# Kernel optimization log

Measured on AMD Instinct MI355X. Metric: run time of the kernel, lower is better.

Reference implementation:

```python
import jax, jax.numpy as jnp
import numpy as np

QC = 12          # effective quantum channels (quantum_channels//4*4)
G = 3            # number of 4-channel quantum groups
DIM = 128
NGROUPS_GN = 8
NUM_LAYER = 1

# PauliZ sign table: wire 0 is the most-significant qubit (PennyLane default.qubit)
_SIGNS = np.array([[1.0 - 2.0 * ((k >> (3 - w)) & 1) for w in range(4)]
                   for k in range(16)], dtype=np.float32)


def _apply_rx(state, phi, w):
    # state: [B,2,2,2,2] complex64; phi: [B]; RX = cos(p/2) I - i sin(p/2) X
    c = jnp.cos(0.5 * phi).astype(jnp.complex64)
    s = (-1j) * jnp.sin(0.5 * phi).astype(jnp.complex64)
    U = jnp.stack([jnp.stack([c, s], -1), jnp.stack([s, c], -1)], -2)  # [B,2,2]
    st = jnp.moveaxis(state, 1 + w, -1)
    st = jnp.einsum('bij,b...j->b...i', U, st)
    return jnp.moveaxis(st, -1, 1 + w)


def _apply_cnot(state, c, t):
    st = jnp.moveaxis(state, (1 + c, 1 + t), (-2, -1))
    st = jnp.concatenate([st[..., 0:1, :], st[..., 1:2, ::-1]], axis=-2)
    return jnp.moveaxis(st, (-2, -1), (1 + c, 1 + t))


def _circuit(x4, theta):
    # AngleEmbedding(RX) + NUM_LAYER x Basic_ansatz; x4: [B,4], theta: [4*NUM_LAYER]
    B = x4.shape[0]
    state = jnp.zeros((B, 2, 2, 2, 2), jnp.complex64).at[:, 0, 0, 0, 0].set(1.0)
    for w in range(4):
        state = _apply_rx(state, x4[:, w], w)
    for l in range(NUM_LAYER):
        th = theta[4 * l:4 * (l + 1)]
        for w in range(4):
            state = _apply_rx(state, jnp.broadcast_to(th[w], (B,)), w)
        for c in range(3):
            state = _apply_cnot(state, c, c + 1)
        state = _apply_cnot(state, 3, 0)
    probs = jnp.abs(state.reshape(B, 16)) ** 2
    return probs @ jnp.asarray(_SIGNS)  # [B,4] PauliZ expvals


def _quantum_block(x_q, qparams):
    # x_q: [B,H,W,QC]; pool spatially, run per-group circuit, broadcast back
    B, H, W, Cq = x_q.shape
    pooled = jnp.mean(x_q, axis=(1, 2)).reshape(B, Cq // 4, 4)
    y = jax.vmap(_circuit, in_axes=(1, 0), out_axes=1)(pooled, qparams)  # [B,G,4]
    y = y.reshape(B, 1, 1, Cq)
    return jnp.broadcast_to(y, (B, H, W, Cq))


def _ws_conv(x, kernel, bias):
    eps = 1e-5  # fp32 branch of WeightStandardizedConv
    mean = jnp.mean(kernel, axis=(0, 1, 2), keepdims=True)
    var = jnp.var(kernel, axis=(0, 1, 2), keepdims=True)
    k = (kernel - mean) / jnp.sqrt(var + eps)
    y = jax.lax.conv_general_dilated(x, k, (1, 1), ((1, 1), (1, 1)),
                                     dimension_numbers=('NHWC', 'HWIO', 'NHWC'))
    return y + bias


def _group_norm(x, scale, bias, groups=NGROUPS_GN, eps=1e-6):
    B, H, W, C = x.shape
    xg = x.reshape(B, H, W, groups, C // groups)
    mu = jnp.mean(xg, axis=(1, 2, 4), keepdims=True)
    var = jnp.var(xg, axis=(1, 2, 4), keepdims=True)
    xn = ((xg - mu) / jnp.sqrt(var + eps)).reshape(B, H, W, C)
    return xn * scale + bias


def setup_inputs() -> dict:
    key = jax.random.key(0)
    ks = jax.random.split(key, 8)
    B, H, W, C, T = 16, 64, 64, DIM, 512
    cc = DIM - QC  # classical conv channels = 116
    return {
        'x': jax.random.normal(ks[0], (B, H, W, C), jnp.float32),
        'time_emb': jax.random.normal(ks[1], (B, T), jnp.float32),
        'qparams': jax.random.uniform(ks[2], (G, 4), jnp.float32),
        'conv0_kernel': jax.random.normal(ks[3], (3, 3, cc, cc), jnp.float32) * 0.05,
        'conv0_bias': jnp.zeros((cc,), jnp.float32),
        'conv1_kernel': jax.random.normal(ks[4], (3, 3, cc, cc), jnp.float32) * 0.05,
        'conv1_bias': jnp.zeros((cc,), jnp.float32),
        'gn0_scale': jnp.ones((C,), jnp.float32),
        'gn0_bias': jnp.zeros((C,), jnp.float32),
        'gn1_scale': jnp.ones((C,), jnp.float32),
        'gn1_bias': jnp.zeros((C,), jnp.float32),
        'time_w': jax.random.normal(ks[5], (T, 2 * DIM), jnp.float32) * 0.02,
        'time_b': jnp.zeros((2 * DIM,), jnp.float32),
    }


def reference(x, time_emb, qparams, conv0_kernel, conv0_bias, conv1_kernel,
              conv1_bias, gn0_scale, gn0_bias, gn1_scale, gn1_bias, time_w, time_b):
    # first quantum + classical branch
    h_q = _quantum_block(x[..., :QC], qparams)
    h_c = _ws_conv(x[..., QC:], conv0_kernel, conv0_bias)
    h = jnp.concatenate([h_q, h_c], axis=-1)
    h = _group_norm(h, gn0_scale, gn0_bias)
    # FiLM conditioning from time embedding
    t = jax.nn.swish(time_emb) @ time_w + time_b  # [B, 2*DIM]
    scale, shift = jnp.split(t[:, None, None, :], 2, axis=-1)
    h = jax.nn.swish(h * (1 + scale) + shift)
    # second quantum + classical branch
    h_q2 = _quantum_block(h[..., :QC], qparams)
    h_c2 = _ws_conv(h[..., QC:], conv1_kernel, conv1_bias)
    h2 = jnp.concatenate([h_q2, h_c2], axis=-1)
    h2 = jax.nn.swish(_group_norm(h2, gn1_scale, gn1_bias))
    return x + h2
```

## Files before the change

kernel.cpp:

```cpp
#include <hip/hip_runtime.h>
#include <math.h>

#define BATCH 16
#define NPX 4096
#define CDIM 128
#define CC 116
#define KTAPS 1044

using u16 = unsigned short;
typedef __attribute__((ext_vector_type(8))) short short8;
typedef __attribute__((ext_vector_type(16))) float f32x16;

__device__ __forceinline__ float swishf(float z) {
    return z / (1.f + __expf(-z));
}
__device__ __forceinline__ float bf2f(u16 u) {
    union { unsigned int i; float f; } v; v.i = ((unsigned int)u) << 16; return v.f;
}
__device__ __forceinline__ u16 f2bf(float f) {
    union { float f; unsigned int i; } v; v.f = f;
    unsigned int r = v.i + 0x7fffu + ((v.i >> 16) & 1u);
    return (u16)(r >> 16);
}

__global__ void k_pre(const float* __restrict__ x, float* __restrict__ part,
                      float* __restrict__ csums) {
    const int bx = blockIdx.x, tid = threadIdx.x;
    if (bx >= 128) {
        int i = (bx - 128) * 256 + tid;
        csums[i * 2] = 0.f;
        csums[i * 2 + 1] = 0.f;
        return;
    }
    const int b = bx >> 3, seg = bx & 7;
    float s[12];
#pragma unroll
    for (int c = 0; c < 12; ++c) s[c] = 0.f;
    const float* xb = x + (size_t)(b * 4096 + seg * 512) * CDIM;
#pragma unroll
    for (int i = 0; i < 2; ++i) {
        const float4* p = (const float4*)(xb + (size_t)(tid + i * 256) * CDIM);
        float4 v0 = p[0], v1 = p[1], v2 = p[2];
        s[0] += v0.x; s[1] += v0.y; s[2] += v0.z; s[3] += v0.w;
        s[4] += v1.x; s[5] += v1.y; s[6] += v1.z; s[7] += v1.w;
        s[8] += v2.x; s[9] += v2.y; s[10] += v2.z; s[11] += v2.w;
    }
    __shared__ float red[12][256];
#pragma unroll
    for (int c = 0; c < 12; ++c) red[c][tid] = s[c];
    __syncthreads();
    for (int st = 128; st > 0; st >>= 1) {
        if (tid < st) {
#pragma unroll
            for (int c = 0; c < 12; ++c) red[c][tid] += red[c][tid + st];
        }
        __syncthreads();
    }
    if (tid < 12) part[bx * 12 + tid] = red[tid][0];
}

__device__ void run_circuit(const float* ang, const float* th, float* z) {
    float ar[16], ai[16];
#pragma unroll
    for (int k = 0; k < 16; ++k) { ar[k] = 0.f; ai[k] = 0.f; }
    ar[0] = 1.f;
#pragma unroll
    for (int pass = 0; pass < 2; ++pass) {
        const float* a = pass ? th : ang;
#pragma unroll
        for (int w = 0; w < 4; ++w) {
            float half = 0.5f * a[w];
            float cth = cosf(half), sth = sinf(half);
            int m = 1 << (3 - w);
#pragma unroll
            for (int k = 0; k < 16; ++k) {
                if (k & m) continue;
                int k2 = k | m;
                float r0 = ar[k], i0 = ai[k], r1 = ar[k2], i1 = ai[k2];
                ar[k]  = cth * r0 + sth * i1;
                ai[k]  = cth * i0 - sth * r1;
                ar[k2] = sth * i0 + cth * r1;
                ai[k2] = -sth * r0 + cth * i1;
            }
        }
    }
#pragma unroll
    for (int e = 0; e < 4; ++e) {
        const int cwi[4] = {0, 1, 2, 3};
        const int twi[4] = {1, 2, 3, 0};
        int mc = 1 << (3 - cwi[e]), mt = 1 << (3 - twi[e]);
#pragma unroll
        for (int k = 0; k < 16; ++k) {
            if ((k & mc) && !(k & mt)) {
                int k2 = k | mt;
                float tr = ar[k]; ar[k] = ar[k2]; ar[k2] = tr;
                float ti = ai[k]; ai[k] = ai[k2]; ai[k2] = ti;
            }
        }
    }
    float zz[4] = {0.f, 0.f, 0.f, 0.f};
#pragma unroll
    for (int k = 0; k < 16; ++k) {
        float p = ar[k] * ar[k] + ai[k] * ai[k];
#pragma unroll
        for (int w = 0; w < 4; ++w) zz[w] += ((k >> (3 - w)) & 1) ? -p : p;
    }
#pragma unroll
    for (int w = 0; w < 4; ++w) z[w] = zz[w];
}

__global__ void k_tw(const float* __restrict__ te, const float* __restrict__ W,
                     const float* __restrict__ tb, float* __restrict__ t,
                     const float* __restrict__ K0, const float* __restrict__ K1,
                     u16* __restrict__ kqp0, u16* __restrict__ kqp1) {
    const int bx = blockIdx.x, tid = threadIdx.x;
    __shared__ float se[512];
    __shared__ float rs[256], rss[256], mb[2];
    if (bx < 16) {
        const int b = bx;
        for (int k = tid; k < 512; k += 256) se[k] = swishf(te[b * 512 + k]);
        __syncthreads();
        float acc = tb[tid];
        for (int k = 0; k < 512; ++k) acc += se[k] * W[k * 256 + tid];
        t[b * 256 + tid] = acc;
        return;
    }
    const int r = bx - 16;
    const float* K = (r >> 7) ? K1 : K0;
    u16* kqp = (r >> 7) ? kqp1 : kqp0;
    const int o = r & 127;
    float s = 0.f, ss = 0.f;
    if (o < CC) {
        for (int idx = tid; idx < KTAPS; idx += 256) {
            float v = K[(size_t)idx * CC + o];
            s += v; ss += v * v;
        }
    }
    rs[tid] = s; rss[tid] = ss;
    __syncthreads();
    for (int st = 128; st > 0; st >>= 1) {
        if (tid < st) { rs[tid] += rs[tid + st]; rss[tid] += rss[tid + st]; }
        __syncthreads();
    }
    if (tid == 0) {
        float m = rs[0] * (1.f / KTAPS);
        float var = rss[0] * (1.f / KTAPS) - m * m;
        mb[0] = m;
        mb[1] = rsqrtf(var + 1e-5f);
    }
    __syncthreads();
    float m = mb[0], inv = mb[1];
    for (int idx = tid; idx < 1152; idx += 256) {
        int tap = idx >> 7, ic = idx & 127;
        float v = 0.f;
        if (o < CC && ic < CC) v = (K[((size_t)tap * CC + ic) * CC + o] - m) * inv;
        int step = tap * 8 + (ic >> 4);
        int lane2 = ((ic >> 3) & 1) * 32 + (o & 31);
        int j = ic & 7;
        kqp[(size_t)(step * 4 + (o >> 5)) * 512 + lane2 * 8 + j] = f2bf(v);
    }
}

template <int MODE>
__launch_bounds__(512, 2)
__global__ void k_conv(const void* __restrict__ inp, const float* __restrict__ Acoef,
                       const float* __restrict__ Bcoef, const u16* __restrict__ kqp,
                       const float* __restrict__ bias, u16* __restrict__ outp,
                       float* __restrict__ csum) {
    __shared__ u16 As[32768];
    __shared__ float cfA[132], cfB[132];
    const int hb = blockIdx.x, b = blockIdx.y;
    const int hp = ((hb & 7) << 2) | (hb >> 3);
    const int h0 = hp * 2;
    const int tid = threadIdx.x, lane = tid & 63, wid = tid >> 6;
    const int wm = wid & 1, wn = wid >> 1;
    const int l31 = lane & 31;
    const int rr = tid >> 8, pp = (tid >> 2) & 63, ck = tid & 3;
    const int swz = (pp & 15) << 4;

    if (MODE == 1) {
        if (tid < 128) {
            int ckk = tid >> 5, ee = tid & 31;
            float a = 0.f, bbv = 0.f;
            if (tid < CC) {
                a = Acoef[b * 128 + 12 + tid];
                bbv = Bcoef[b * 128 + 12 + tid];
            }
            cfA[ckk * 33 + ee] = a;
            cfB[ckk * 33 + ee] = bbv;
        }
    }

    float fv[32]; short8 sv[4];

#define LOADCHUNK(r, val) do { \
    const int hi_ = h0 + (r) - 1; \
    val = (hi_ >= 0 && hi_ < 64); \
    if (val) { \
        const size_t px_ = (size_t)((b * 64 + hi_) * 64 + pp); \
        if (MODE == 0) { \
            const float* sp_ = (const float*)inp + px_ * 128 + 12 + ck * 32; \
            if (ck < 3) { \
                _Pragma("unroll") for (int j = 0; j < 8; ++j) *(float4*)&fv[j * 4] = ((const float4*)sp_)[j]; \
            } else { \
                _Pragma("unroll") for (int j = 0; j < 5; ++j) *(float4*)&fv[j * 4] = ((const float4*)sp_)[j]; \
                _Pragma("unroll") for (int e = 20; e < 32; ++e) fv[e] = 0.f; \
            } \
        } else { \
            const u16* sp_ = (const u16*)inp + px_ * 128 + ck * 32; \
            _Pragma("unroll") for (int k = 0; k < 4; ++k) sv[k] = ((const short8*)sp_)[k]; \
        } \
    } \
} while (0)

#define WRITECHUNK(r, val) do { \
    u16 t_[32]; \
    if (val) { \
        if (MODE == 0) { \
            _Pragma("unroll") for (int e = 0; e < 32; ++e) t_[e] = f2bf(fv[e]); \
        } else { \
            _Pragma("unroll") for (int e = 0; e < 32; ++e) { \
                int c_ = ck * 32 + e; \
                float f_ = bf2f((u16)sv[e >> 3][e & 7]); \
                float w_ = swishf(f_ * cfA[ck * 33 + e] + cfB[ck * 33 + e]); \
                t_[e] = (c_ < CC) ? f2bf(w_) : (u16)0; \
            } \
        } \
    } else { \
        _Pragma("unroll") for (int e = 0; e < 32; ++e) t_[e] = 0; \
    } \
    char* rb_ = (char*)As + ((r) * 64 + pp) * 256; \
    _Pragma("unroll") for (int k = 0; k < 4; ++k) \
        *(short8*)(rb_ + ((ck * 64 + k * 16) ^ swz)) = *(const short8*)&t_[k * 8]; \
} while (0)

    bool valA, valC;
    LOADCHUNK(rr, valA);
    if (MODE == 1) __syncthreads();
    WRITECHUNK(rr, valA);
    LOADCHUNK(2 + rr, valC);

    const u16* bp = kqp + (size_t)wn * 512 + (size_t)lane * 8;
    short8 breg[4];
#pragma unroll
    for (int s = 0; s < 4; ++s) breg[s] = *(const short8*)(bp + ((size_t)s << 11));

    const int kh16 = (lane >> 5) << 4;
    int coloff[2][3], colswz[2][3];
#pragma unroll
    for (int mf = 0; mf < 2; ++mf)
#pragma unroll
        for (int q = 0; q < 3; ++q) {
            int c = mf * 32 + l31 + q - 1;
            int cc = c < 0 ? 0 : (c > 63 ? 63 : c);
            coloff[mf][q] = cc << 7;
            colswz[mf][q] = (cc & 15) << 4;
        }
    const bool e0 = (l31 == 0), e1 = (l31 == 31);
    const short8 zero8 = {0, 0, 0, 0, 0, 0, 0, 0};
    const int rowb = wm * 8192;

    asm volatile("s_waitcnt lgkmcnt(0)" ::: "memory");
    __builtin_amdgcn_s_barrier();

    f32x16 acc[2];
#pragma unroll
    for (int mf = 0; mf < 2; ++mf)
#pragma unroll
        for (int r = 0; r < 16; ++r) acc[mf][r] = 0.f;

#define AREAD(dst, s) do { \
    const int tap_ = (s) >> 3, p_ = tap_ / 3, q_ = tap_ % 3; \
    const int chb_ = ((s) & 7) << 5; \
    dst[0] = *(const short8*)&As[rowb + p_ * 8192 + coloff[0][q_] + (((chb_ + kh16) ^ colswz[0][q_]) >> 1)]; \
    dst[1] = *(const short8*)&As[rowb + p_ * 8192 + coloff[1][q_] + (((chb_ + kh16) ^ colswz[1][q_]) >> 1)]; \
} while (0)

#define STEP(s, base, lim) do { \
    const int cur_ = ((s) - (base)) & 1, nxt_ = cur_ ^ 1; \
    if ((s) + 1 < (lim)) AREAD(afr[nxt_], (s) + 1); \
    const int q_ = ((s) >> 3) % 3; \
    short8 a0_ = afr[cur_][0], a1_ = afr[cur_][1]; \
    if (q_ == 0) a0_ = e0 ? zero8 : a0_; \
    if (q_ == 2) a1_ = e1 ? zero8 : a1_; \
    __builtin_amdgcn_s_setprio(1); \
    acc[0] = __builtin_amdgcn_mfma_f32_32x32x16_bf16(a0_, breg[(s) & 3], acc[0], 0, 0, 0); \
    acc[1] = __builtin_amdgcn_mfma_f32_32x32x16_bf16(a1_, breg[(s) & 3], acc[1], 0, 0, 0); \
    __builtin_amdgcn_s_setprio(0); \
    if ((s) + 4 < 72) breg[(s) & 3] = *(const short8*)(bp + ((size_t)((s) + 4) << 11)); \
} while (0)

    short8 afr[2][2];
    AREAD(afr[0], 0);
#pragma unroll
    for (int s = 0; s < 24; ++s) STEP(s, 0, 24);

    WRITECHUNK(2 + rr, valC);
    asm volatile("s_waitcnt lgkmcnt(0)" ::: "memory");
    __builtin_amdgcn_s_barrier();

    AREAD(afr[0], 24);
#pragma unroll
    for (int s = 24; s < 72; ++s) STEP(s, 24, 72);

    const int oc = wn * 32 + l31;
    const float bv = (oc < CC) ? bias[oc] : 0.f;
    float cs = 0.f, cq = 0.f;
    const int rbase = (lane >> 5) << 2;

    asm volatile("s_waitcnt lgkmcnt(0)" ::: "memory");
    __builtin_amdgcn_s_barrier();
#pragma unroll
    for (int mf = 0; mf < 2; ++mf) {
#pragma unroll
        for (int r = 0; r < 16; ++r) {
            int drow = (r & 3) + ((r >> 2) << 3) + rbase;
            int flat = wm * 64 + mf * 32 + drow;
            float v = acc[mf][r] + bv;
            As[flat * 128 + oc] = f2bf(v);
            cs += v;
            cq += v * v;
        }
    }
    asm volatile("s_waitcnt lgkmcnt(0)" ::: "memory");
    __builtin_amdgcn_s_barrier();
    {
        size_t obase = (size_t)(b * 4096 + h0 * 64) * 128;
#pragma unroll
        for (int k = 0; k < 4; ++k)
            *(short8*)&outp[obase + k * 4096 + tid * 8] = *(const short8*)&As[k * 4096 + tid * 8];
    }
    cs += __shfl_xor(cs, 32);
    cq += __shfl_xor(cq, 32);
    if (lane < 32) {
        atomicAdd(&csum[(b * 128 + oc) * 2], cs);
        atomicAdd(&csum[(b * 128 + oc) * 2 + 1], cq);
    }
#undef LOADCHUNK
#undef WRITECHUNK
#undef AREAD
#undef STEP
}

__global__ void k_mid0(const float* __restrict__ part, const float* __restrict__ csum,
                       const float* __restrict__ t, const float* __restrict__ gs,
                       const float* __restrict__ gb, const float* __restrict__ qp,
                       float* __restrict__ A, float* __restrict__ Bc,
                       float* __restrict__ y2) {
    __shared__ float pooled_s[192], y1s[192], sst[128][2];
    int tid = threadIdx.x;
    if (tid < 192) {
        int b = tid / 12, c = tid % 12;
        float s = 0.f;
#pragma unroll
        for (int k = 0; k < 8; ++k) s += part[(b * 8 + k) * 12 + c];
        pooled_s[tid] = s * (1.f / 4096.f);
    }
    __syncthreads();
    if (tid < 48) {
        int b = tid / 3, g = tid % 3;
        float z[4];
        run_circuit(&pooled_s[b * 12 + g * 4], qp + g * 4, z);
#pragma unroll
        for (int w = 0; w < 4; ++w) y1s[b * 12 + g * 4 + w] = z[w];
    }
    __syncthreads();
    if (tid < 128) {
        int b = tid >> 3, g = tid & 7;
        float S = 0.f, SS = 0.f;
#pragma unroll
        for (int e = 0; e < 16; ++e) {
            int orig = g * 16 + e;
            if (orig >= 12) {
                int cc = orig - 12;
                S += csum[(b * 128 + cc) * 2];
                SS += csum[(b * 128 + cc) * 2 + 1];
            }
        }
        if (g == 0) {
#pragma unroll
            for (int c = 0; c < 12; ++c) {
                float v = y1s[b * 12 + c];
                S += 4096.f * v;
                SS += 4096.f * v * v;
            }
        }
        float mu = S * (1.f / 65536.f);
        float var = SS * (1.f / 65536.f) - mu * mu;
        sst[tid][0] = mu;
        sst[tid][1] = rsqrtf(var + 1e-6f);
    }
    __syncthreads();
    for (int i = tid; i < 2048; i += 256) {
        int b = i >> 7, c = i & 127, g = c >> 4;
        float mu = sst[b * 8 + g][0], isd = sst[b * 8 + g][1];
        float sc = t[b * 256 + c], sh = t[b * 256 + 128 + c];
        float a = isd * gs[c];
        float bb = gb[c] - mu * a;
        A[i] = a * (1.f + sc);
        Bc[i] = bb * (1.f + sc) + sh;
    }
    if (tid < 48) {
        int b = tid / 3, gq = tid % 3;
        float pin[4], z[4];
        float mu = sst[b * 8][0], isd = sst[b * 8][1];
#pragma unroll
        for (int w = 0; w < 4; ++w) {
            int c = gq * 4 + w;
            float a = isd * gs[c];
            float bb = gb[c] - mu * a;
            float sc = t[b * 256 + c], sh = t[b * 256 + 128 + c];
            float v = y1s[b * 12 + c];
            pin[w] = swishf(v * (a * (1.f + sc)) + (bb * (1.f + sc) + sh));
        }
        run_circuit(pin, qp + gq * 4, z);
#pragma unroll
        for (int w = 0; w < 4; ++w) y2[b * 12 + gq * 4 + w] = z[w];
    }
}

__global__ void k_mid1(const float* __restrict__ csum, const float* __restrict__ y2,
                       const float* __restrict__ gs, const float* __restrict__ gb,
                       float* __restrict__ A2, float* __restrict__ B2,
                       float* __restrict__ oq) {
    __shared__ float sst[128][2];
    int tid = threadIdx.x;
    if (tid < 128) {
        int b = tid >> 3, g = tid & 7;
        float S = 0.f, SS = 0.f;
#pragma unroll
        for (int e = 0; e < 16; ++e) {
            int orig = g * 16 + e;
            if (orig >= 12) {
                int cc = orig - 12;
                S += csum[(b * 128 + cc) * 2];
                SS += csum[(b * 128 + cc) * 2 + 1];
            }
        }
        if (g == 0) {
#pragma unroll
            for (int c = 0; c < 12; ++c) {
                float v = y2[b * 12 + c];
                S += 4096.f * v;
                SS += 4096.f * v * v;
            }
        }
        float mu = S * (1.f / 65536.f);
        float var = SS * (1.f / 65536.f) - mu * mu;
        sst[tid][0] = mu;
        sst[tid][1] = rsqrtf(var + 1e-6f);
    }
    __syncthreads();
    for (int i = tid; i < 2048; i += 256) {
        int b = i >> 7, c = i & 127, g = c >> 4;
        float mu = sst[b * 8 + g][0], isd = sst[b * 8 + g][1];
        float a = isd * gs[c];
        A2[i] = a;
        B2[i] = gb[c] - mu * a;
    }
    if (tid < 192) {
        int b = tid / 12, c = tid % 12;
        float mu = sst[b * 8][0], isd = sst[b * 8][1];
        float a = isd * gs[c];
        float bb = gb[c] - mu * a;
        oq[b * 12 + c] = swishf(y2[b * 12 + c] * a + bb);
    }
}

__global__ void k_final(const float* __restrict__ x, const u16* __restrict__ co,
                        const float* __restrict__ A2, const float* __restrict__ B2,
                        const float* __restrict__ oq, float* __restrict__ outp) {
    const int t = blockIdx.x, b = blockIdx.y;
    const int seg = t >> 6, hraw = t & 63;
    const int h = ((hraw & 7) << 3) | (hraw >> 3);
    const int tid = threadIdx.x;
    const size_t px = (size_t)(b * 64 + h) * 64 + seg * 8 + (tid >> 5);
    const int c4 = tid & 31, c = c4 * 4;
    float4 xv = *(const float4*)(x + px * CDIM + c);
    float4 r;
    if (c4 < 3) {
        const float* q = oq + b * 12 + c;
        r.x = xv.x + q[0]; r.y = xv.y + q[1]; r.z = xv.z + q[2]; r.w = xv.w + q[3];
    } else {
        int cc = c - 12;
        const u16* hp = co + px * 128 + cc;
        float4 a = *(const float4*)(A2 + b * 128 + c);
        float4 bb = *(const float4*)(B2 + b * 128 + c);
        r.x = xv.x + swishf(bf2f(hp[0]) * a.x + bb.x);
        r.y = xv.y + swishf(bf2f(hp[1]) * a.y + bb.y);
        r.z = xv.z + swishf(bf2f(hp[2]) * a.z + bb.z);
        r.w = xv.w + swishf(bf2f(hp[3]) * a.w + bb.w);
    }
    *(float4*)(outp + px * CDIM + c) = r;
}

extern "C" void kernel_launch(void* const* d_in, const int* in_sizes, int n_in,
                              void* d_out, int out_size, void* d_ws, size_t ws_size,
                              hipStream_t stream) {
    const float* x        = (const float*)d_in[0];
    const float* time_emb = (const float*)d_in[1];
    const float* qparams  = (const float*)d_in[2];
    const float* c0k      = (const float*)d_in[3];
    const float* c0b      = (const float*)d_in[4];
    const float* c1k      = (const float*)d_in[5];
    const float* c1b      = (const float*)d_in[6];
    const float* g0s      = (const float*)d_in[7];
    const float* g0b      = (const float*)d_in[8];
    const float* g1s      = (const float*)d_in[9];
    const float* g1b      = (const float*)d_in[10];
    const float* tw       = (const float*)d_in[11];
    const float* tb       = (const float*)d_in[12];
    float* outp = (float*)d_out;
    float* ws = (float*)d_ws;

    size_t o = 0;
    auto alloc = [&](size_t n) { size_t r = o; o += (n + 15) & ~(size_t)15; return r; };
    float* part   = ws + alloc(1536);
    float* csums  = ws + alloc(8192);
    float* csum0  = csums;
    float* csum1  = csums + 4096;
    float* t      = ws + alloc(4096);
    float* A      = ws + alloc(2048);
    float* Bc     = ws + alloc(2048);
    float* A2     = ws + alloc(2048);
    float* B2     = ws + alloc(2048);
    float* y2     = ws + alloc(192);
    float* oq     = ws + alloc(192);
    u16* kqp0     = (u16*)(ws + alloc(73728));
    u16* kqp1     = (u16*)(ws + alloc(73728));
    u16* convA    = (u16*)(ws + alloc(4194304));
    u16* convB    = (u16*)(ws + alloc(4194304));

    k_pre<<<144, 256, 0, stream>>>(x, part, csums);
    k_tw<<<272, 256, 0, stream>>>(time_emb, tw, tb, t, c0k, c1k, kqp0, kqp1);

    dim3 cgrid(32, 16);
    k_conv<0><<<cgrid, 512, 0, stream>>>(x, nullptr, nullptr, kqp0, c0b, convA, csum0);
    k_mid0<<<1, 256, 0, stream>>>(part, csum0, t, g0s, g0b, qparams, A, Bc, y2);

    k_conv<1><<<cgrid, 512, 0, stream>>>(convA, A, Bc, kqp1, c1b, convB, csum1);
    k_mid1<<<1, 256, 0, stream>>>(csum1, y2, g1s, g1b, A2, B2, oq);
    k_final<<<dim3(512, 16), 256, 0, stream>>>(x, convB, A2, B2, oq, outp);
}
```

Measured before the change: 120.3 us.

## Shrink conv tile to one output row per block and merge prologue kernels

```diff
diff --git a/kernel.cpp b/kernel.cpp
--- a/kernel.cpp
+++ b/kernel.cpp
@@ -21,42 +21,6 @@
     union { float f; unsigned int i; } v; v.f = f;
     unsigned int r = v.i + 0x7fffu + ((v.i >> 16) & 1u);
     return (u16)(r >> 16);
-}
-
-__global__ void k_pre(const float* __restrict__ x, float* __restrict__ part,
-                      float* __restrict__ csums) {
-    const int bx = blockIdx.x, tid = threadIdx.x;
-    if (bx >= 128) {
-        int i = (bx - 128) * 256 + tid;
-        csums[i * 2] = 0.f;
-        csums[i * 2 + 1] = 0.f;
-        return;
-    }
-    const int b = bx >> 3, seg = bx & 7;
-    float s[12];
-#pragma unroll
-    for (int c = 0; c < 12; ++c) s[c] = 0.f;
-    const float* xb = x + (size_t)(b * 4096 + seg * 512) * CDIM;
-#pragma unroll
-    for (int i = 0; i < 2; ++i) {
-        const float4* p = (const float4*)(xb + (size_t)(tid + i * 256) * CDIM);
-        float4 v0 = p[0], v1 = p[1], v2 = p[2];
-        s[0] += v0.x; s[1] += v0.y; s[2] += v0.z; s[3] += v0.w;
-        s[4] += v1.x; s[5] += v1.y; s[6] += v1.z; s[7] += v1.w;
-        s[8] += v2.x; s[9] += v2.y; s[10] += v2.z; s[11] += v2.w;
-    }
-    __shared__ float red[12][256];
-#pragma unroll
-    for (int c = 0; c < 12; ++c) red[c][tid] = s[c];
-    __syncthreads();
-    for (int st = 128; st > 0; st >>= 1) {
-        if (tid < st) {
-#pragma unroll
-            for (int c = 0; c < 12; ++c) red[c][tid] += red[c][tid + st];
-        }
-        __syncthreads();
-    }
-    if (tid < 12) part[bx * 12 + tid] = red[tid][0];
 }
 
 __device__ void run_circuit(const float* ang, const float* th, float* z) {
@@ -109,15 +73,51 @@
     for (int w = 0; w < 4; ++w) z[w] = zz[w];
 }
 
-__global__ void k_tw(const float* __restrict__ te, const float* __restrict__ W,
-                     const float* __restrict__ tb, float* __restrict__ t,
-                     const float* __restrict__ K0, const float* __restrict__ K1,
-                     u16* __restrict__ kqp0, u16* __restrict__ kqp1) {
+__global__ void k_misc(const float* __restrict__ x, float* __restrict__ part,
+                       float* __restrict__ csums,
+                       const float* __restrict__ te, const float* __restrict__ W,
+                       const float* __restrict__ tb, float* __restrict__ t,
+                       const float* __restrict__ K0, const float* __restrict__ K1,
+                       u16* __restrict__ kqp0, u16* __restrict__ kqp1) {
     const int bx = blockIdx.x, tid = threadIdx.x;
+    __shared__ float red[12][256];
     __shared__ float se[512];
     __shared__ float rs[256], rss[256], mb[2];
-    if (bx < 16) {
-        const int b = bx;
+    if (bx < 128) {
+        const int b = bx >> 3, seg = bx & 7;
+        float s[12];
+#pragma unroll
+        for (int c = 0; c < 12; ++c) s[c] = 0.f;
+        const float* xb = x + (size_t)(b * 4096 + seg * 512) * CDIM;
+#pragma unroll
+        for (int i = 0; i < 2; ++i) {
+            const float4* p = (const float4*)(xb + (size_t)(tid + i * 256) * CDIM);
+            float4 v0 = p[0], v1 = p[1], v2 = p[2];
+            s[0] += v0.x; s[1] += v0.y; s[2] += v0.z; s[3] += v0.w;
+            s[4] += v1.x; s[5] += v1.y; s[6] += v1.z; s[7] += v1.w;
+            s[8] += v2.x; s[9] += v2.y; s[10] += v2.z; s[11] += v2.w;
+        }
+#pragma unroll
+        for (int c = 0; c < 12; ++c) red[c][tid] = s[c];
+        __syncthreads();
+        for (int st = 128; st > 0; st >>= 1) {
+            if (tid < st) {
+#pragma unroll
+                for (int c = 0; c < 12; ++c) red[c][tid] += red[c][tid + st];
+            }
+            __syncthreads();
+        }
+        if (tid < 12) part[bx * 12 + tid] = red[tid][0];
+        return;
+    }
+    if (bx < 144) {
+        int i = (bx - 128) * 256 + tid;
+        csums[i * 2] = 0.f;
+        csums[i * 2 + 1] = 0.f;
+        return;
+    }
+    if (bx < 160) {
+        const int b = bx - 144;
         for (int k = tid; k < 512; k += 256) se[k] = swishf(te[b * 512 + k]);
         __syncthreads();
         float acc = tb[tid];
@@ -125,7 +125,7 @@
         t[b * 256 + tid] = acc;
         return;
     }
-    const int r = bx - 16;
+    const int r = bx - 160;
     const float* K = (r >> 7) ? K1 : K0;
     u16* kqp = (r >> 7) ? kqp1 : kqp0;
     const int o = r & 127;
@@ -162,39 +162,32 @@
 }
 
 template <int MODE>
-__launch_bounds__(512, 2)
+__launch_bounds__(512, 6)
 __global__ void k_conv(const void* __restrict__ inp, const float* __restrict__ Acoef,
                        const float* __restrict__ Bcoef, const u16* __restrict__ kqp,
                        const float* __restrict__ bias, u16* __restrict__ outp,
                        float* __restrict__ csum) {
-    __shared__ u16 As[32768];
+    __shared__ u16 As[3 * 64 * 128];
     __shared__ float cfA[132], cfB[132];
     const int hb = blockIdx.x, b = blockIdx.y;
-    const int hp = ((hb & 7) << 2) | (hb >> 3);
-    const int h0 = hp * 2;
+    const int h = ((hb & 7) << 3) | (hb >> 3);
     const int tid = threadIdx.x, lane = tid & 63, wid = tid >> 6;
-    const int wm = wid & 1, wn = wid >> 1;
+    const int mh = wid >> 2, ng = wid & 3;
     const int l31 = lane & 31;
-    const int rr = tid >> 8, pp = (tid >> 2) & 63, ck = tid & 3;
+    const int r1 = tid >> 8, pp = (tid >> 2) & 63, ck = tid & 3;
     const int swz = (pp & 15) << 4;
 
     if (MODE == 1) {
-        if (tid < 128) {
-            int ckk = tid >> 5, ee = tid & 31;
-            float a = 0.f, bbv = 0.f;
-            if (tid < CC) {
-                a = Acoef[b * 128 + 12 + tid];
-                bbv = Bcoef[b * 128 + 12 + tid];
-            }
-            cfA[ckk * 33 + ee] = a;
-            cfB[ckk * 33 + ee] = bbv;
-        }
-    }
-
-    float fv[32]; short8 sv[4];
-
-#define LOADCHUNK(r, val) do { \
-    const int hi_ = h0 + (r) - 1; \
+        if (tid < CC) {
+            cfA[(tid >> 5) * 33 + (tid & 31)] = Acoef[b * 128 + 12 + tid];
+            cfB[(tid >> 5) * 33 + (tid & 31)] = Bcoef[b * 128 + 12 + tid];
+        }
+    }
+
+    float fvA[32], fvC[32]; short8 svA[4], svC[4];
+
+#define LOADCHUNK(r, fv, sv, val) do { \
+    const int hi_ = h + (r) - 1; \
     val = (hi_ >= 0 && hi_ < 64); \
     if (val) { \
         const size_t px_ = (size_t)((b * 64 + hi_) * 64 + pp); \
@@ -213,7 +206,7 @@
     } \
 } while (0)
 
-#define WRITECHUNK(r, val) do { \
+#define WRITECHUNK(r, fv, sv, val) do { \
     u16 t_[32]; \
     if (val) { \
         if (MODE == 0) { \
@@ -234,76 +227,70 @@
         *(short8*)(rb_ + ((ck * 64 + k * 16) ^ swz)) = *(const short8*)&t_[k * 8]; \
 } while (0)
 
-    bool valA, valC;
-    LOADCHUNK(rr, valA);
+    bool valA, valC = false;
+    LOADCHUNK(r1, fvA, svA, valA);
+    if (tid < 256) LOADCHUNK(2, fvC, svC, valC);
     if (MODE == 1) __syncthreads();
-    WRITECHUNK(rr, valA);
-    LOADCHUNK(2 + rr, valC);
-
-    const u16* bp = kqp + (size_t)wn * 512 + (size_t)lane * 8;
-    short8 breg[4];
-#pragma unroll
-    for (int s = 0; s < 4; ++s) breg[s] = *(const short8*)(bp + ((size_t)s << 11));
+    WRITECHUNK(r1, fvA, svA, valA);
+
+    const u16* bp = kqp + (size_t)ng * 512 + (size_t)lane * 8;
+    short8 breg[3];
+#pragma unroll
+    for (int s = 0; s < 3; ++s) breg[s] = *(const short8*)(bp + ((size_t)s << 11));
 
     const int kh16 = (lane >> 5) << 4;
-    int coloff[2][3], colswz[2][3];
-#pragma unroll
-    for (int mf = 0; mf < 2; ++mf)
-#pragma unroll
-        for (int q = 0; q < 3; ++q) {
-            int c = mf * 32 + l31 + q - 1;
-            int cc = c < 0 ? 0 : (c > 63 ? 63 : c);
-            coloff[mf][q] = cc << 7;
-            colswz[mf][q] = (cc & 15) << 4;
-        }
-    const bool e0 = (l31 == 0), e1 = (l31 == 31);
+    int coloff[3], colswz[3];
+#pragma unroll
+    for (int q = 0; q < 3; ++q) {
+        int c = mh * 32 + l31 + q - 1;
+        int cc = c < 0 ? 0 : (c > 63 ? 63 : c);
+        coloff[q] = cc << 7;
+        colswz[q] = (cc & 15) << 4;
+    }
+    const bool e0 = (mh == 0) && (l31 == 0);
+    const bool e1 = (mh == 1) && (l31 == 31);
     const short8 zero8 = {0, 0, 0, 0, 0, 0, 0, 0};
-    const int rowb = wm * 8192;
 
     asm volatile("s_waitcnt lgkmcnt(0)" ::: "memory");
     __builtin_amdgcn_s_barrier();
 
-    f32x16 acc[2];
-#pragma unroll
-    for (int mf = 0; mf < 2; ++mf)
-#pragma unroll
-        for (int r = 0; r < 16; ++r) acc[mf][r] = 0.f;
+    f32x16 acc;
+#pragma unroll
+    for (int r = 0; r < 16; ++r) acc[r] = 0.f;
 
 #define AREAD(dst, s) do { \
     const int tap_ = (s) >> 3, p_ = tap_ / 3, q_ = tap_ % 3; \
     const int chb_ = ((s) & 7) << 5; \
-    dst[0] = *(const short8*)&As[rowb + p_ * 8192 + coloff[0][q_] + (((chb_ + kh16) ^ colswz[0][q_]) >> 1)]; \
-    dst[1] = *(const short8*)&As[rowb + p_ * 8192 + coloff[1][q_] + (((chb_ + kh16) ^ colswz[1][q_]) >> 1)]; \
+    dst = *(const short8*)&As[p_ * 8192 + coloff[q_] + (((chb_ + kh16) ^ colswz[q_]) >> 1)]; \
 } while (0)
 
 #define STEP(s, base, lim) do { \
     const int cur_ = ((s) - (base)) & 1, nxt_ = cur_ ^ 1; \
     if ((s) + 1 < (lim)) AREAD(afr[nxt_], (s) + 1); \
     const int q_ = ((s) >> 3) % 3; \
-    short8 a0_ = afr[cur_][0], a1_ = afr[cur_][1]; \
-    if (q_ == 0) a0_ = e0 ? zero8 : a0_; \
-    if (q_ == 2) a1_ = e1 ? zero8 : a1_; \
+    short8 a_ = afr[cur_]; \
+    if (q_ == 0) a_ = e0 ? zero8 : a_; \
+    if (q_ == 2) a_ = e1 ? zero8 : a_; \
     __builtin_amdgcn_s_setprio(1); \
-    acc[0] = __builtin_amdgcn_mfma_f32_32x32x16_bf16(a0_, breg[(s) & 3], acc[0], 0, 0, 0); \
-    acc[1] = __builtin_amdgcn_mfma_f32_32x32x16_bf16(a1_, breg[(s) & 3], acc[1], 0, 0, 0); \
+    acc = __builtin_amdgcn_mfma_f32_32x32x16_bf16(a_, breg[(s) % 3], acc, 0, 0, 0); \
     __builtin_amdgcn_s_setprio(0); \
-    if ((s) + 4 < 72) breg[(s) & 3] = *(const short8*)(bp + ((size_t)((s) + 4) << 11)); \
+    if ((s) + 3 < 72) breg[(s) % 3] = *(const short8*)(bp + ((size_t)((s) + 3) << 11)); \
 } while (0)
 
-    short8 afr[2][2];
+    short8 afr[2];
     AREAD(afr[0], 0);
 #pragma unroll
-    for (int s = 0; s < 24; ++s) STEP(s, 0, 24);
-
-    WRITECHUNK(2 + rr, valC);
+    for (int s = 0; s < 48; ++s) STEP(s, 0, 48);
+
+    if (tid < 256) WRITECHUNK(2, fvC, svC, valC);
     asm volatile("s_waitcnt lgkmcnt(0)" ::: "memory");
     __builtin_amdgcn_s_barrier();
 
-    AREAD(afr[0], 24);
-#pragma unroll
-    for (int s = 24; s < 72; ++s) STEP(s, 24, 72);
-
-    const int oc = wn * 32 + l31;
+    AREAD(afr[0], 48);
+#pragma unroll
+    for (int s = 48; s < 72; ++s) STEP(s, 48, 72);
+
+    const int oc = ng * 32 + l31;
     const float bv = (oc < CC) ? bias[oc] : 0.f;
     float cs = 0.f, cq = 0.f;
     const int rbase = (lane >> 5) << 2;
@@ -311,23 +298,20 @@
     asm volatile("s_waitcnt lgkmcnt(0)" ::: "memory");
     __builtin_amdgcn_s_barrier();
 #pragma unroll
-    for (int mf = 0; mf < 2; ++mf) {
-#pragma unroll
-        for (int r = 0; r < 16; ++r) {
-            int drow = (r & 3) + ((r >> 2) << 3) + rbase;
-            int flat = wm * 64 + mf * 32 + drow;
-            float v = acc[mf][r] + bv;
-            As[flat * 128 + oc] = f2bf(v);
-            cs += v;
-            cq += v * v;
-        }
+    for (int r = 0; r < 16; ++r) {
+        int row = (r & 3) + ((r >> 2) << 3) + rbase;
+        int px = mh * 32 + row;
+        float v = acc[r] + bv;
+        As[px * 128 + oc] = f2bf(v);
+        cs += v;
+        cq += v * v;
     }
     asm volatile("s_waitcnt lgkmcnt(0)" ::: "memory");
     __builtin_amdgcn_s_barrier();
     {
-        size_t obase = (size_t)(b * 4096 + h0 * 64) * 128;
-#pragma unroll
-        for (int k = 0; k < 4; ++k)
+        size_t obase = (size_t)(b * 4096 + h * 64) * 128;
+#pragma unroll
+        for (int k = 0; k < 2; ++k)
             *(short8*)&outp[obase + k * 4096 + tid * 8] = *(const short8*)&As[k * 4096 + tid * 8];
     }
     cs += __shfl_xor(cs, 32);
@@ -531,10 +515,10 @@
     u16* convA    = (u16*)(ws + alloc(4194304));
     u16* convB    = (u16*)(ws + alloc(4194304));
 
-    k_pre<<<144, 256, 0, stream>>>(x, part, csums);
-    k_tw<<<272, 256, 0, stream>>>(time_emb, tw, tb, t, c0k, c1k, kqp0, kqp1);
-
-    dim3 cgrid(32, 16);
+    k_misc<<<416, 256, 0, stream>>>(x, part, csums, time_emb, tw, tb, t,
+                                    c0k, c1k, kqp0, kqp1);
+
+    dim3 cgrid(64, 16);
     k_conv<0><<<cgrid, 512, 0, stream>>>(x, nullptr, nullptr, kqp0, c0b, convA, csum0);
     k_mid0<<<1, 256, 0, stream>>>(part, csum0, t, g0s, g0b, qparams, A, Bc, y2);
 
```

New measurement: 163.6 us. 1.36x slower.

## Merge prep kernels, fold mid1 into final, and simplify conv LDS addressing

Applied to the files above, without the earlier changes.

```diff
diff --git a/kernel.cpp b/kernel.cpp
--- a/kernel.cpp
+++ b/kernel.cpp
@@ -21,42 +21,6 @@
     union { float f; unsigned int i; } v; v.f = f;
     unsigned int r = v.i + 0x7fffu + ((v.i >> 16) & 1u);
     return (u16)(r >> 16);
-}
-
-__global__ void k_pre(const float* __restrict__ x, float* __restrict__ part,
-                      float* __restrict__ csums) {
-    const int bx = blockIdx.x, tid = threadIdx.x;
-    if (bx >= 128) {
-        int i = (bx - 128) * 256 + tid;
-        csums[i * 2] = 0.f;
-        csums[i * 2 + 1] = 0.f;
-        return;
-    }
-    const int b = bx >> 3, seg = bx & 7;
-    float s[12];
-#pragma unroll
-    for (int c = 0; c < 12; ++c) s[c] = 0.f;
-    const float* xb = x + (size_t)(b * 4096 + seg * 512) * CDIM;
-#pragma unroll
-    for (int i = 0; i < 2; ++i) {
-        const float4* p = (const float4*)(xb + (size_t)(tid + i * 256) * CDIM);
-        float4 v0 = p[0], v1 = p[1], v2 = p[2];
-        s[0] += v0.x; s[1] += v0.y; s[2] += v0.z; s[3] += v0.w;
-        s[4] += v1.x; s[5] += v1.y; s[6] += v1.z; s[7] += v1.w;
-        s[8] += v2.x; s[9] += v2.y; s[10] += v2.z; s[11] += v2.w;
-    }
-    __shared__ float red[12][256];
-#pragma unroll
-    for (int c = 0; c < 12; ++c) red[c][tid] = s[c];
-    __syncthreads();
-    for (int st = 128; st > 0; st >>= 1) {
-        if (tid < st) {
-#pragma unroll
-            for (int c = 0; c < 12; ++c) red[c][tid] += red[c][tid + st];
-        }
-        __syncthreads();
-    }
-    if (tid < 12) part[bx * 12 + tid] = red[tid][0];
 }
 
 __device__ void run_circuit(const float* ang, const float* th, float* z) {
@@ -109,15 +73,51 @@
     for (int w = 0; w < 4; ++w) z[w] = zz[w];
 }
 
-__global__ void k_tw(const float* __restrict__ te, const float* __restrict__ W,
-                     const float* __restrict__ tb, float* __restrict__ t,
-                     const float* __restrict__ K0, const float* __restrict__ K1,
-                     u16* __restrict__ kqp0, u16* __restrict__ kqp1) {
+__global__ void k_misc(const float* __restrict__ x, float* __restrict__ part,
+                       float* __restrict__ csums,
+                       const float* __restrict__ te, const float* __restrict__ W,
+                       const float* __restrict__ tb, float* __restrict__ t,
+                       const float* __restrict__ K0, const float* __restrict__ K1,
+                       u16* __restrict__ kqp0, u16* __restrict__ kqp1) {
     const int bx = blockIdx.x, tid = threadIdx.x;
+    __shared__ float red[12][256];
     __shared__ float se[512];
     __shared__ float rs[256], rss[256], mb[2];
-    if (bx < 16) {
-        const int b = bx;
+    if (bx < 128) {
+        const int b = bx >> 3, seg = bx & 7;
+        float s[12];
+#pragma unroll
+        for (int c = 0; c < 12; ++c) s[c] = 0.f;
+        const float* xb = x + (size_t)(b * 4096 + seg * 512) * CDIM;
+#pragma unroll
+        for (int i = 0; i < 2; ++i) {
+            const float4* p = (const float4*)(xb + (size_t)(tid + i * 256) * CDIM);
+            float4 v0 = p[0], v1 = p[1], v2 = p[2];
+            s[0] += v0.x; s[1] += v0.y; s[2] += v0.z; s[3] += v0.w;
+            s[4] += v1.x; s[5] += v1.y; s[6] += v1.z; s[7] += v1.w;
+            s[8] += v2.x; s[9] += v2.y; s[10] += v2.z; s[11] += v2.w;
+        }
+#pragma unroll
+        for (int c = 0; c < 12; ++c) red[c][tid] = s[c];
+        __syncthreads();
+        for (int st = 128; st > 0; st >>= 1) {
+            if (tid < st) {
+#pragma unroll
+                for (int c = 0; c < 12; ++c) red[c][tid] += red[c][tid + st];
+            }
+            __syncthreads();
+        }
+        if (tid < 12) part[bx * 12 + tid] = red[tid][0];
+        return;
+    }
+    if (bx < 144) {
+        int i = (bx - 128) * 256 + tid;
+        csums[i * 2] = 0.f;
+        csums[i * 2 + 1] = 0.f;
+        return;
+    }
+    if (bx < 160) {
+        const int b = bx - 144;
         for (int k = tid; k < 512; k += 256) se[k] = swishf(te[b * 512 + k]);
         __syncthreads();
         float acc = tb[tid];
@@ -125,7 +125,7 @@
         t[b * 256 + tid] = acc;
         return;
     }
-    const int r = bx - 16;
+    const int r = bx - 160;
     const float* K = (r >> 7) ? K1 : K0;
     u16* kqp = (r >> 7) ? kqp1 : kqp0;
     const int o = r & 127;
@@ -189,6 +189,7 @@
             cfA[ckk * 33 + ee] = a;
             cfB[ckk * 33 + ee] = bbv;
         }
+        __syncthreads();
     }
 
     float fv[32]; short8 sv[4];
@@ -236,29 +237,29 @@
 
     bool valA, valC;
     LOADCHUNK(rr, valA);
-    if (MODE == 1) __syncthreads();
     WRITECHUNK(rr, valA);
     LOADCHUNK(2 + rr, valC);
 
-    const u16* bp = kqp + (size_t)wn * 512 + (size_t)lane * 8;
+    uintptr_t bub = (uintptr_t)(kqp + (size_t)wn * 512);
+    unsigned int blo = __builtin_amdgcn_readfirstlane((unsigned int)bub);
+    unsigned int bhi = __builtin_amdgcn_readfirstlane((unsigned int)(bub >> 32));
+    const u16* bpS = (const u16*)((((unsigned long long)bhi) << 32) | blo);
+    const int lane8 = lane * 8;
     short8 breg[4];
 #pragma unroll
-    for (int s = 0; s < 4; ++s) breg[s] = *(const short8*)(bp + ((size_t)s << 11));
+    for (int s = 0; s < 4; ++s) breg[s] = *(const short8*)(bpS + ((size_t)s << 11) + lane8);
 
     const int kh16 = (lane >> 5) << 4;
-    int coloff[2][3], colswz[2][3];
-#pragma unroll
-    for (int mf = 0; mf < 2; ++mf)
-#pragma unroll
-        for (int q = 0; q < 3; ++q) {
-            int c = mf * 32 + l31 + q - 1;
-            int cc = c < 0 ? 0 : (c > 63 ? 63 : c);
-            coloff[mf][q] = cc << 7;
-            colswz[mf][q] = (cc & 15) << 4;
-        }
+    int V0[3], V1[3];
+#pragma unroll
+    for (int q = 0; q < 3; ++q) {
+        int c0 = l31 + q - 1;       c0 = c0 < 0 ? 0 : c0;
+        int c1 = 32 + l31 + q - 1;  c1 = c1 > 63 ? 63 : c1;
+        V0[q] = wm * 16384 + (c0 << 8) + (kh16 ^ ((c0 & 15) << 4));
+        V1[q] = wm * 16384 + (c1 << 8) + (kh16 ^ ((c1 & 15) << 4));
+    }
     const bool e0 = (l31 == 0), e1 = (l31 == 31);
     const short8 zero8 = {0, 0, 0, 0, 0, 0, 0, 0};
-    const int rowb = wm * 8192;
 
     asm volatile("s_waitcnt lgkmcnt(0)" ::: "memory");
     __builtin_amdgcn_s_barrier();
@@ -272,8 +273,8 @@
 #define AREAD(dst, s) do { \
     const int tap_ = (s) >> 3, p_ = tap_ / 3, q_ = tap_ % 3; \
     const int chb_ = ((s) & 7) << 5; \
-    dst[0] = *(const short8*)&As[rowb + p_ * 8192 + coloff[0][q_] + (((chb_ + kh16) ^ colswz[0][q_]) >> 1)]; \
-    dst[1] = *(const short8*)&As[rowb + p_ * 8192 + coloff[1][q_] + (((chb_ + kh16) ^ colswz[1][q_]) >> 1)]; \
+    dst[0] = *(const short8*)((const char*)As + ((V0[q_] ^ chb_) + p_ * 16384)); \
+    dst[1] = *(const short8*)((const char*)As + ((V1[q_] ^ chb_) + p_ * 16384)); \
 } while (0)
 
 #define STEP(s, base, lim) do { \
@@ -287,7 +288,7 @@
     acc[0] = __builtin_amdgcn_mfma_f32_32x32x16_bf16(a0_, breg[(s) & 3], acc[0], 0, 0, 0); \
     acc[1] = __builtin_amdgcn_mfma_f32_32x32x16_bf16(a1_, breg[(s) & 3], acc[1], 0, 0, 0); \
     __builtin_amdgcn_s_setprio(0); \
-    if ((s) + 4 < 72) breg[(s) & 3] = *(const short8*)(bp + ((size_t)((s) + 4) << 11)); \
+    if ((s) + 4 < 72) breg[(s) & 3] = *(const short8*)(bpS + ((size_t)((s) + 4) << 11) + lane8); \
 } while (0)
 
     short8 afr[2][2];
@@ -419,14 +420,17 @@
     }
 }
 
-__global__ void k_mid1(const float* __restrict__ csum, const float* __restrict__ y2,
-                       const float* __restrict__ gs, const float* __restrict__ gb,
-                       float* __restrict__ A2, float* __restrict__ B2,
-                       float* __restrict__ oq) {
-    __shared__ float sst[128][2];
-    int tid = threadIdx.x;
-    if (tid < 128) {
-        int b = tid >> 3, g = tid & 7;
+__global__ void k_final(const float* __restrict__ x, const u16* __restrict__ co,
+                        const float* __restrict__ csum, const float* __restrict__ y2,
+                        const float* __restrict__ gs, const float* __restrict__ gb,
+                        float* __restrict__ outp) {
+    __shared__ float sst[8][2];
+    const int t = blockIdx.x, b = blockIdx.y;
+    const int seg = t >> 6, hraw = t & 63;
+    const int h = ((hraw & 7) << 3) | (hraw >> 3);
+    const int tid = threadIdx.x;
+    if (tid < 8) {
+        const int g = tid;
         float S = 0.f, SS = 0.f;
 #pragma unroll
         for (int e = 0; e < 16; ++e) {
@@ -447,49 +451,33 @@
         }
         float mu = S * (1.f / 65536.f);
         float var = SS * (1.f / 65536.f) - mu * mu;
-        sst[tid][0] = mu;
-        sst[tid][1] = rsqrtf(var + 1e-6f);
+        sst[g][0] = mu;
+        sst[g][1] = rsqrtf(var + 1e-6f);
     }
     __syncthreads();
-    for (int i = tid; i < 2048; i += 256) {
-        int b = i >> 7, c = i & 127, g = c >> 4;
-        float mu = sst[b * 8 + g][0], isd = sst[b * 8 + g][1];
-        float a = isd * gs[c];
-        A2[i] = a;
-        B2[i] = gb[c] - mu * a;
-    }
-    if (tid < 192) {
-        int b = tid / 12, c = tid % 12;
-        float mu = sst[b * 8][0], isd = sst[b * 8][1];
-        float a = isd * gs[c];
-        float bb = gb[c] - mu * a;
-        oq[b * 12 + c] = swishf(y2[b * 12 + c] * a + bb);
-    }
-}
-
-__global__ void k_final(const float* __restrict__ x, const u16* __restrict__ co,
-                        const float* __restrict__ A2, const float* __restrict__ B2,
-                        const float* __restrict__ oq, float* __restrict__ outp) {
-    const int t = blockIdx.x, b = blockIdx.y;
-    const int seg = t >> 6, hraw = t & 63;
-    const int h = ((hraw & 7) << 3) | (hraw >> 3);
-    const int tid = threadIdx.x;
     const size_t px = (size_t)(b * 64 + h) * 64 + seg * 8 + (tid >> 5);
     const int c4 = tid & 31, c = c4 * 4;
+    const int g = c >> 4;
+    const float mu = sst[g][0], isd = sst[g][1];
+    float4 gsv = *(const float4*)(gs + c);
+    float4 gbv = *(const float4*)(gb + c);
+    float a0 = isd * gsv.x, a1 = isd * gsv.y, a2 = isd * gsv.z, a3 = isd * gsv.w;
+    float b0 = gbv.x - mu * a0, b1 = gbv.y - mu * a1;
+    float b2 = gbv.z - mu * a2, b3 = gbv.w - mu * a3;
     float4 xv = *(const float4*)(x + px * CDIM + c);
     float4 r;
     if (c4 < 3) {
-        const float* q = oq + b * 12 + c;
-        r.x = xv.x + q[0]; r.y = xv.y + q[1]; r.z = xv.z + q[2]; r.w = xv.w + q[3];
+        const float* q = y2 + b * 12 + c;
+        r.x = xv.x + swishf(q[0] * a0 + b0);
+        r.y = xv.y + swishf(q[1] * a1 + b1);
+        r.z = xv.z + swishf(q[2] * a2 + b2);
+        r.w = xv.w + swishf(q[3] * a3 + b3);
     } else {
-        int cc = c - 12;
-        const u16* hp = co + px * 128 + cc;
-        float4 a = *(const float4*)(A2 + b * 128 + c);
-        float4 bb = *(const float4*)(B2 + b * 128 + c);
-        r.x = xv.x + swishf(bf2f(hp[0]) * a.x + bb.x);
-        r.y = xv.y + swishf(bf2f(hp[1]) * a.y + bb.y);
-        r.z = xv.z + swishf(bf2f(hp[2]) * a.z + bb.z);
-        r.w = xv.w + swishf(bf2f(hp[3]) * a.w + bb.w);
+        const u16* hp = co + px * 128 + (c - 12);
+        r.x = xv.x + swishf(bf2f(hp[0]) * a0 + b0);
+        r.y = xv.y + swishf(bf2f(hp[1]) * a1 + b1);
+        r.z = xv.z + swishf(bf2f(hp[2]) * a2 + b2);
+        r.w = xv.w + swishf(bf2f(hp[3]) * a3 + b3);
     }
     *(float4*)(outp + px * CDIM + c) = r;
 }
@@ -522,23 +510,19 @@
     float* t      = ws + alloc(4096);
     float* A      = ws + alloc(2048);
     float* Bc     = ws + alloc(2048);
-    float* A2     = ws + alloc(2048);
-    float* B2     = ws + alloc(2048);
     float* y2     = ws + alloc(192);
-    float* oq     = ws + alloc(192);
     u16* kqp0     = (u16*)(ws + alloc(73728));
     u16* kqp1     = (u16*)(ws + alloc(73728));
     u16* convA    = (u16*)(ws + alloc(4194304));
     u16* convB    = (u16*)(ws + alloc(4194304));
 
-    k_pre<<<144, 256, 0, stream>>>(x, part, csums);
-    k_tw<<<272, 256, 0, stream>>>(time_emb, tw, tb, t, c0k, c1k, kqp0, kqp1);
+    k_misc<<<416, 256, 0, stream>>>(x, part, csums, time_emb, tw, tb, t,
+                                    c0k, c1k, kqp0, kqp1);
 
     dim3 cgrid(32, 16);
     k_conv<0><<<cgrid, 512, 0, stream>>>(x, nullptr, nullptr, kqp0, c0b, convA, csum0);
     k_mid0<<<1, 256, 0, stream>>>(part, csum0, t, g0s, g0b, qparams, A, Bc, y2);
 
     k_conv<1><<<cgrid, 512, 0, stream>>>(convA, A, Bc, kqp1, c1b, convB, csum1);
-    k_mid1<<<1, 256, 0, stream>>>(csum1, y2, g1s, g1b, A2, B2, oq);
-    k_final<<<dim3(512, 16), 256, 0, stream>>>(x, convB, A2, B2, oq, outp);
-}
+    k_final<<<dim3(512, 16), 256, 0, stream>>>(x, convB, csum1, y2, g1s, g1b, outp);
+}
```

Result: slower. 125.8 us (+4.6%).
